# Kernel optimization log

Measured on AMD Instinct MI355X. Metric: run time of the kernel, lower is better.

## Reference

```python
import jax, jax.numpy as jnp
import numpy as np

NUM_STEPS = 5  # DVF2DDF(num_steps=5)


def _warp(vol, ddf, mode):
    """MONAI Warp: sample vol at (voxel index + ddf), align_corners=True, zeros padding.
    vol: [N,C,D,H,W]; ddf: [N,3,D,H,W] (channels = d,h,w displacement)."""
    N, C, D, H, W = vol.shape
    gd, gh, gw = jnp.meshgrid(jnp.arange(D, dtype=ddf.dtype),
                              jnp.arange(H, dtype=ddf.dtype),
                              jnp.arange(W, dtype=ddf.dtype), indexing='ij')
    cd = gd + ddf[:, 0]  # [N,D,H,W] absolute sample coords
    ch = gh + ddf[:, 1]
    cw = gw + ddf[:, 2]
    vol_flat = vol.reshape(N, C, D * H * W)

    def gather(di, hi, wi, valid):
        dc = jnp.clip(di, 0, D - 1)
        hc = jnp.clip(hi, 0, H - 1)
        wc = jnp.clip(wi, 0, W - 1)
        flat = ((dc * H + hc) * W + wc).reshape(N, 1, -1)
        v = jnp.take_along_axis(vol_flat, flat, axis=2).reshape(N, C, D, H, W)
        return v * valid[:, None]

    def in_bounds(di, hi, wi):
        return ((di >= 0) & (di < D) & (hi >= 0) & (hi < H)
                & (wi >= 0) & (wi < W)).astype(vol.dtype)

    if mode == 'nearest':
        di = jnp.round(cd).astype(jnp.int32)
        hi = jnp.round(ch).astype(jnp.int32)
        wi = jnp.round(cw).astype(jnp.int32)
        return gather(di, hi, wi, in_bounds(di, hi, wi))

    # trilinear ('bilinear' in grid_sample naming)
    d0 = jnp.floor(cd); h0 = jnp.floor(ch); w0 = jnp.floor(cw)
    fd = cd - d0; fh = ch - h0; fw = cw - w0
    d0i = d0.astype(jnp.int32); h0i = h0.astype(jnp.int32); w0i = w0.astype(jnp.int32)
    out = jnp.zeros_like(vol)
    for dd in (0, 1):
        for dh in (0, 1):
            for dw in (0, 1):
                di = d0i + dd; hi = h0i + dh; wi = w0i + dw
                wgt = ((fd if dd else 1 - fd)
                       * (fh if dh else 1 - fh)
                       * (fw if dw else 1 - fw))
                out = out + gather(di, hi, wi, in_bounds(di, hi, wi)) * wgt[:, None]
    return out


def _dvf2ddf(dvf, num_steps=NUM_STEPS):
    """Scaling-and-squaring integration of a stationary velocity field (MONAI DVF2DDF)."""
    ddf = dvf / (2 ** num_steps)
    for _ in range(num_steps):
        ddf = ddf + _warp(ddf, ddf, 'bilinear')
    return ddf


def setup_inputs() -> dict:
    key = jax.random.key(0)
    ks = jax.random.split(key, 6)
    D = H = W = 160
    return {
        "dvf0": jax.random.normal(ks[0], (1, 3, D, H, W), jnp.float32),
        "dvf1": jax.random.normal(ks[1], (1, 3, D, H, W), jnp.float32),
        "image": jax.random.normal(ks[2], (1, 1, D, H, W), jnp.float32),
        "cavity": jax.random.randint(ks[3], (1, 1, D, H, W), 0, 5, jnp.int32),
        "coronary": jax.random.randint(ks[4], (1, 1, D, H, W), 0, 3, jnp.int32),
        "w": jax.random.uniform(ks[5], (), jnp.float32),
    }


def reference(dvf0, dvf1, image, cavity, coronary, w):
    # linear blend of the two neighbouring phase DVFs
    dvf = dvf0 * (1 - w) + dvf1 * w
    ddf = _dvf2ddf(dvf)
    img_warped = _warp(image, ddf, 'bilinear')
    # labels are concatenated along batch and warped with nearest, ddf repeated
    labels = jnp.concatenate([cavity, coronary], axis=0).astype(jnp.float32)  # [2,1,D,H,W]
    lab_warped = _warp(labels, jnp.tile(ddf, (2, 1, 1, 1, 1)), 'nearest')
    cav_warped = lab_warped[0][None].astype(jnp.uint8)
    cor_warped = lab_warped[1][None].astype(jnp.uint8)
    return img_warped, cav_warped, cor_warped, ddf
```

## Files before the change

kernel.cpp:

```cpp
#include <hip/hip_runtime.h>

#define DD 160
#define HH 160
#define WW 160
#define PL (HH*WW)
#define S (DD*PL)

__device__ __forceinline__ float fmul(float a, float b){ return __fmul_rn(a,b); }
__device__ __forceinline__ float fadd(float a, float b){ return __fadd_rn(a,b); }
__device__ __forceinline__ float fsub(float a, float b){ return __fsub_rn(a,b); }

__global__ __launch_bounds__(256) void init_kernel(const float* __restrict__ dvf0,
                                                   const float* __restrict__ dvf1,
                                                   const float* __restrict__ wp,
                                                   float* __restrict__ outi) {
    int p = (blockIdx.x * 256 + threadIdx.x) * 4;
    float w = wp[0];
    float onew = fsub(1.0f, w);
    float a0[4], a1[4], a2[4], b0[4], b1[4], b2[4];
    *(float4*)a0 = *(const float4*)(dvf0 + p);
    *(float4*)a1 = *(const float4*)(dvf0 + S + p);
    *(float4*)a2 = *(const float4*)(dvf0 + 2 * S + p);
    *(float4*)b0 = *(const float4*)(dvf1 + p);
    *(float4*)b1 = *(const float4*)(dvf1 + S + p);
    *(float4*)b2 = *(const float4*)(dvf1 + 2 * S + p);
    float o[12];
    #pragma unroll
    for (int j = 0; j < 4; ++j) {
        o[3*j]   = fmul(fadd(fmul(a0[j], onew), fmul(b0[j], w)), 0.03125f);
        o[3*j+1] = fmul(fadd(fmul(a1[j], onew), fmul(b1[j], w)), 0.03125f);
        o[3*j+2] = fmul(fadd(fmul(a2[j], onew), fmul(b2[j], w)), 0.03125f);
    }
    float* dst = outi + (size_t)3 * p;
    *(float4*)(dst)     = *(float4*)(o);
    *(float4*)(dst + 4) = *(float4*)(o + 4);
    *(float4*)(dst + 8) = *(float4*)(o + 8);
}

template<bool PLANAR>
__global__ __launch_bounds__(256) void warp_step(const float* __restrict__ in,
                                                 float* __restrict__ out) {
    int b  = (blockIdx.x & 7) * 1000 + (blockIdx.x >> 3);
    int ix = b % 5;
    int r  = b / 5;
    int iy = r % 20;
    int iz = r / 20;
    int lane = threadIdx.x & 63, wid = threadIdx.x >> 6;
    int x  = (ix << 5) | (lane & 31);
    int y  = (iy << 3) | (wid << 1) | (lane >> 5);
    int z0 = iz << 1;
    int p0 = (z0 * HH + y) * WW + x;

    float ctr[2][3];
    #pragma unroll
    for (int j = 0; j < 2; ++j) {
        const float* src = in + (size_t)3 * (p0 + j * PL);
        ctr[j][0] = src[0]; ctr[j][1] = src[1]; ctr[j][2] = src[2];
    }

    #pragma unroll
    for (int j = 0; j < 2; ++j) {
        int z = z0 + j;
        int p = p0 + j * PL;
        float vd = ctr[j][0], vh = ctr[j][1], vw = ctr[j][2];
        float cd = fadd((float)z, vd);
        float ch = fadd((float)y, vh);
        float cw = fadd((float)x, vw);

        float d0 = floorf(cd), h0 = floorf(ch), w0 = floorf(cw);
        float fd = fsub(cd, d0), fh = fsub(ch, h0), fw = fsub(cw, w0);
        float gd = fsub(1.0f, fd), gh = fsub(1.0f, fh), gw = fsub(1.0f, fw);
        int d0i = (int)d0, h0i = (int)h0, w0i = (int)w0;

        int   qa[8];
        float wt[8];
        #pragma unroll
        for (int t = 0; t < 8; ++t) {
            int dd = t >> 2, dh = (t >> 1) & 1, dw = t & 1;
            int di = d0i + dd, hi = h0i + dh, wi = w0i + dw;
            bool valid = (di >= 0) & (di < DD) & (hi >= 0) & (hi < HH)
                       & (wi >= 0) & (wi < WW);
            float wgt = fmul(fmul(dd ? fd : gd, dh ? fh : gh), dw ? fw : gw);
            wt[t] = valid ? wgt : 0.0f;
            int dc = min(max(di, 0), DD - 1);
            int hc = min(max(hi, 0), HH - 1);
            int wc = min(max(wi, 0), WW - 1);
            qa[t] = 3 * ((dc * HH + hc) * WW + wc);
        }
        float g[8][3];
        #pragma unroll
        for (int t = 0; t < 8; ++t) {
            g[t][0] = in[qa[t]];
            g[t][1] = in[qa[t] + 1];
            g[t][2] = in[qa[t] + 2];
        }
        float acc0 = 0.0f, acc1 = 0.0f, acc2 = 0.0f;
        #pragma unroll
        for (int t = 0; t < 8; ++t) {
            acc0 = fadd(acc0, fmul(g[t][0], wt[t]));
            acc1 = fadd(acc1, fmul(g[t][1], wt[t]));
            acc2 = fadd(acc2, fmul(g[t][2], wt[t]));
        }
        float r0 = fadd(vd, acc0);
        float r1 = fadd(vh, acc1);
        float r2 = fadd(vw, acc2);

        if (PLANAR) {
            out[p] = r0; out[S + p] = r1; out[2 * S + p] = r2;
        } else {
            float* dst = out + (size_t)3 * p;
            dst[0] = r0; dst[1] = r1; dst[2] = r2;
        }
    }
}

__global__ __launch_bounds__(256) void final_kernel(const float* __restrict__ ddf,
                                                    const float* __restrict__ image,
                                                    const int* __restrict__ cav,
                                                    const int* __restrict__ cor,
                                                    float* __restrict__ out) {
    int b  = (blockIdx.x & 7) * 1000 + (blockIdx.x >> 3);
    int ix = b % 5;
    int r  = b / 5;
    int iy = r % 20;
    int iz = r / 20;
    int lane = threadIdx.x & 63, wid = threadIdx.x >> 6;
    int x  = (ix << 5) | (lane & 31);
    int y  = (iy << 3) | (wid << 1) | (lane >> 5);
    int z0 = iz << 1;
    int p0 = (z0 * HH + y) * WW + x;

    float dzs[2], dhs[2], dws[2];
    #pragma unroll
    for (int j = 0; j < 2; ++j) {
        dzs[j] = ddf[p0 + j * PL];
        dhs[j] = ddf[S + p0 + j * PL];
        dws[j] = ddf[2 * S + p0 + j * PL];
    }

    #pragma unroll
    for (int j = 0; j < 2; ++j) {
        int z = z0 + j;
        int p = p0 + j * PL;
        float cd = fadd((float)z, dzs[j]);
        float ch = fadd((float)y, dhs[j]);
        float cw = fadd((float)x, dws[j]);

        float d0 = floorf(cd), h0 = floorf(ch), w0 = floorf(cw);
        float fd = fsub(cd, d0), fh = fsub(ch, h0), fw = fsub(cw, w0);
        float gd = fsub(1.0f, fd), gh = fsub(1.0f, fh), gw = fsub(1.0f, fw);
        int d0i = (int)d0, h0i = (int)h0, w0i = (int)w0;

        int   qa[8];
        float wt[8];
        #pragma unroll
        for (int t = 0; t < 8; ++t) {
            int dd = t >> 2, dh = (t >> 1) & 1, dw = t & 1;
            int di = d0i + dd, hi = h0i + dh, wi = w0i + dw;
            bool valid = (di >= 0) & (di < DD) & (hi >= 0) & (hi < HH)
                       & (wi >= 0) & (wi < WW);
            float wgt = fmul(fmul(dd ? fd : gd, dh ? fh : gh), dw ? fw : gw);
            wt[t] = valid ? wgt : 0.0f;
            int dc = min(max(di, 0), DD - 1);
            int hc = min(max(hi, 0), HH - 1);
            int wc = min(max(wi, 0), WW - 1);
            qa[t] = (dc * HH + hc) * WW + wc;
        }
        float g[8];
        #pragma unroll
        for (int t = 0; t < 8; ++t) g[t] = image[qa[t]];
        float acc = 0.0f;
        #pragma unroll
        for (int t = 0; t < 8; ++t) acc = fadd(acc, fmul(g[t], wt[t]));
        out[p] = acc;

        int di = (int)rintf(cd), hi = (int)rintf(ch), wi = (int)rintf(cw);
        bool valid = (di >= 0) & (di < DD) & (hi >= 0) & (hi < HH)
                   & (wi >= 0) & (wi < WW);
        int dc = min(max(di, 0), DD - 1);
        int hc = min(max(hi, 0), HH - 1);
        int wc = min(max(wi, 0), WW - 1);
        int q = (dc * HH + hc) * WW + wc;
        out[S + p]     = valid ? (float)cav[q] : 0.0f;
        out[2 * S + p] = valid ? (float)cor[q] : 0.0f;
    }
}

extern "C" void kernel_launch(void* const* d_in, const int* in_sizes, int n_in,
                              void* d_out, int out_size, void* d_ws, size_t ws_size,
                              hipStream_t stream) {
    const float* dvf0   = (const float*)d_in[0];
    const float* dvf1   = (const float*)d_in[1];
    const float* image  = (const float*)d_in[2];
    const int*   cav    = (const int*)d_in[3];
    const int*   cor    = (const int*)d_in[4];
    const float* w      = (const float*)d_in[5];

    float* out  = (float*)d_out;
    float* bufA = out;
    float* bufB = out + (size_t)3 * S;

    init_kernel<<<4000, 256, 0, stream>>>(dvf0, dvf1, w, bufA);
    warp_step<false><<<8000, 256, 0, stream>>>(bufA, bufB);
    warp_step<false><<<8000, 256, 0, stream>>>(bufB, bufA);
    warp_step<false><<<8000, 256, 0, stream>>>(bufA, bufB);
    warp_step<false><<<8000, 256, 0, stream>>>(bufB, bufA);
    warp_step<true ><<<8000, 256, 0, stream>>>(bufA, bufB);
    final_kernel<<<8000, 256, 0, stream>>>(bufB, image, cav, cor, bufA);
}
```

Measured before the change: 412.5 us.

## Pad displacement field to float4 and pack image/labels for single gathers

Intermediate displacement fields are stored as padded float4 (AoS with a dummy lane) in workspace and output buffers, so each trilinear corner fetch is one 16-byte load instead of three scalar loads. The final warp packs image, cavity and coronary into a float4 volume, so one gather serves both trilinear image sampling and nearest label lookup. The nearest label is chosen from the eight trilinear corners by comparing the rounded index with the floor index. This costs extra workspace, a pack pass, and a third more bytes per voxel. If the workspace is too small, the old path is used.

```diff
diff --git a/kernel.cpp b/kernel.cpp
--- a/kernel.cpp
+++ b/kernel.cpp
@@ -9,6 +9,188 @@
 __device__ __forceinline__ float fmul(float a, float b){ return __fmul_rn(a,b); }
 __device__ __forceinline__ float fadd(float a, float b){ return __fadd_rn(a,b); }
 __device__ __forceinline__ float fsub(float a, float b){ return __fsub_rn(a,b); }
+
+
+__global__ __launch_bounds__(256) void init4_kernel(const float* __restrict__ dvf0,
+                                                    const float* __restrict__ dvf1,
+                                                    const float* __restrict__ wp,
+                                                    float4* __restrict__ outi) {
+    int p = (blockIdx.x * 256 + threadIdx.x) * 4;
+    float w = wp[0];
+    float onew = fsub(1.0f, w);
+    float a0[4], a1[4], a2[4], b0[4], b1[4], b2[4];
+    *(float4*)a0 = *(const float4*)(dvf0 + p);
+    *(float4*)a1 = *(const float4*)(dvf0 + S + p);
+    *(float4*)a2 = *(const float4*)(dvf0 + 2 * S + p);
+    *(float4*)b0 = *(const float4*)(dvf1 + p);
+    *(float4*)b1 = *(const float4*)(dvf1 + S + p);
+    *(float4*)b2 = *(const float4*)(dvf1 + 2 * S + p);
+    #pragma unroll
+    for (int j = 0; j < 4; ++j) {
+        float o0 = fmul(fadd(fmul(a0[j], onew), fmul(b0[j], w)), 0.03125f);
+        float o1 = fmul(fadd(fmul(a1[j], onew), fmul(b1[j], w)), 0.03125f);
+        float o2 = fmul(fadd(fmul(a2[j], onew), fmul(b2[j], w)), 0.03125f);
+        outi[p + j] = make_float4(o0, o1, o2, 0.0f);
+    }
+}
+
+template<bool PLANAR>
+__global__ __launch_bounds__(256) void warp_step4(const float4* __restrict__ in,
+                                                  float4* __restrict__ out4,
+                                                  float* __restrict__ outp) {
+    int b  = (blockIdx.x & 7) * 1000 + (blockIdx.x >> 3);
+    int ix = b % 5;
+    int r  = b / 5;
+    int iy = r % 20;
+    int iz = r / 20;
+    int lane = threadIdx.x & 63, wid = threadIdx.x >> 6;
+    int x  = (ix << 5) | (lane & 31);
+    int y  = (iy << 3) | (wid << 1) | (lane >> 5);
+    int z0 = iz << 1;
+    int p0 = (z0 * HH + y) * WW + x;
+
+    float4 ctr[2];
+    ctr[0] = in[p0];
+    ctr[1] = in[p0 + PL];
+
+    #pragma unroll
+    for (int j = 0; j < 2; ++j) {
+        int z = z0 + j;
+        int p = p0 + j * PL;
+        float vd = ctr[j].x, vh = ctr[j].y, vw = ctr[j].z;
+        float cd = fadd((float)z, vd);
+        float ch = fadd((float)y, vh);
+        float cw = fadd((float)x, vw);
+
+        float d0 = floorf(cd), h0 = floorf(ch), w0 = floorf(cw);
+        float fd = fsub(cd, d0), fh = fsub(ch, h0), fw = fsub(cw, w0);
+        float gd = fsub(1.0f, fd), gh = fsub(1.0f, fh), gw = fsub(1.0f, fw);
+        int d0i = (int)d0, h0i = (int)h0, w0i = (int)w0;
+
+        int   qa[8];
+        float wt[8];
+        #pragma unroll
+        for (int t = 0; t < 8; ++t) {
+            int dd = t >> 2, dh = (t >> 1) & 1, dw = t & 1;
+            int di = d0i + dd, hi = h0i + dh, wi = w0i + dw;
+            bool valid = (di >= 0) & (di < DD) & (hi >= 0) & (hi < HH)
+                       & (wi >= 0) & (wi < WW);
+            float wgt = fmul(fmul(dd ? fd : gd, dh ? fh : gh), dw ? fw : gw);
+            wt[t] = valid ? wgt : 0.0f;
+            int dc = min(max(di, 0), DD - 1);
+            int hc = min(max(hi, 0), HH - 1);
+            int wc = min(max(wi, 0), WW - 1);
+            qa[t] = (dc * HH + hc) * WW + wc;
+        }
+        float4 g[8];
+        #pragma unroll
+        for (int t = 0; t < 8; ++t) g[t] = in[qa[t]];
+
+        float acc0 = 0.0f, acc1 = 0.0f, acc2 = 0.0f;
+        #pragma unroll
+        for (int t = 0; t < 8; ++t) {
+            acc0 = fadd(acc0, fmul(g[t].x, wt[t]));
+            acc1 = fadd(acc1, fmul(g[t].y, wt[t]));
+            acc2 = fadd(acc2, fmul(g[t].z, wt[t]));
+        }
+        float r0 = fadd(vd, acc0);
+        float r1 = fadd(vh, acc1);
+        float r2 = fadd(vw, acc2);
+
+        if (PLANAR) {
+            outp[p] = r0; outp[S + p] = r1; outp[2 * S + p] = r2;
+        } else {
+            out4[p] = make_float4(r0, r1, r2, 0.0f);
+        }
+    }
+}
+
+__global__ __launch_bounds__(256) void pack_kernel(const float* __restrict__ img,
+                                                   const int* __restrict__ cav,
+                                                   const int* __restrict__ cor,
+                                                   float4* __restrict__ out) {
+    int p = (blockIdx.x * 256 + threadIdx.x) * 4;
+    float im[4]; int cv[4]; int co[4];
+    *(float4*)im = *(const float4*)(img + p);
+    *(int4*)cv   = *(const int4*)(cav + p);
+    *(int4*)co   = *(const int4*)(cor + p);
+    #pragma unroll
+    for (int j = 0; j < 4; ++j)
+        out[p + j] = make_float4(im[j], (float)cv[j], (float)co[j], 0.0f);
+}
+
+__global__ __launch_bounds__(256) void final4_kernel(const float* __restrict__ ddf,
+                                                     const float4* __restrict__ packed,
+                                                     float* __restrict__ out) {
+    int b  = (blockIdx.x & 7) * 1000 + (blockIdx.x >> 3);
+    int ix = b % 5;
+    int r  = b / 5;
+    int iy = r % 20;
+    int iz = r / 20;
+    int lane = threadIdx.x & 63, wid = threadIdx.x >> 6;
+    int x  = (ix << 5) | (lane & 31);
+    int y  = (iy << 3) | (wid << 1) | (lane >> 5);
+    int z0 = iz << 1;
+    int p0 = (z0 * HH + y) * WW + x;
+
+    float dzs[2], dhs[2], dws[2];
+    #pragma unroll
+    for (int j = 0; j < 2; ++j) {
+        dzs[j] = ddf[p0 + j * PL];
+        dhs[j] = ddf[S + p0 + j * PL];
+        dws[j] = ddf[2 * S + p0 + j * PL];
+    }
+
+    #pragma unroll
+    for (int j = 0; j < 2; ++j) {
+        int z = z0 + j;
+        int p = p0 + j * PL;
+        float cd = fadd((float)z, dzs[j]);
+        float ch = fadd((float)y, dhs[j]);
+        float cw = fadd((float)x, dws[j]);
+
+        float d0 = floorf(cd), h0 = floorf(ch), w0 = floorf(cw);
+        float fd = fsub(cd, d0), fh = fsub(ch, h0), fw = fsub(cw, w0);
+        float gd = fsub(1.0f, fd), gh = fsub(1.0f, fh), gw = fsub(1.0f, fw);
+        int d0i = (int)d0, h0i = (int)h0, w0i = (int)w0;
+
+        int   qa[8];
+        float wt[8];
+        #pragma unroll
+        for (int t = 0; t < 8; ++t) {
+            int dd = t >> 2, dh = (t >> 1) & 1, dw = t & 1;
+            int di = d0i + dd, hi = h0i + dh, wi = w0i + dw;
+            bool valid = (di >= 0) & (di < DD) & (hi >= 0) & (hi < HH)
+                       & (wi >= 0) & (wi < WW);
+            float wgt = fmul(fmul(dd ? fd : gd, dh ? fh : gh), dw ? fw : gw);
+            wt[t] = valid ? wgt : 0.0f;
+            int dc = min(max(di, 0), DD - 1);
+            int hc = min(max(hi, 0), HH - 1);
+            int wc = min(max(wi, 0), WW - 1);
+            qa[t] = (dc * HH + hc) * WW + wc;
+        }
+        float4 g[8];
+        #pragma unroll
+        for (int t = 0; t < 8; ++t) g[t] = packed[qa[t]];
+
+        float acc = 0.0f;
+        #pragma unroll
+        for (int t = 0; t < 8; ++t) acc = fadd(acc, fmul(g[t].x, wt[t]));
+        out[p] = acc;
+
+        int rd = (int)rintf(cd), rh = (int)rintf(ch), rw = (int)rintf(cw);
+        bool vn = (rd >= 0) & (rd < DD) & (rh >= 0) & (rh < HH)
+                & (rw >= 0) & (rw < WW);
+        bool b2 = (rd != d0i), b1 = (rh != h0i), b0 = (rw != w0i);
+        float cavv = b2 ? (b1 ? (b0 ? g[7].y : g[6].y) : (b0 ? g[5].y : g[4].y))
+                        : (b1 ? (b0 ? g[3].y : g[2].y) : (b0 ? g[1].y : g[0].y));
+        float corv = b2 ? (b1 ? (b0 ? g[7].z : g[6].z) : (b0 ? g[5].z : g[4].z))
+                        : (b1 ? (b0 ? g[3].z : g[2].z) : (b0 ? g[1].z : g[0].z));
+        out[S + p]     = vn ? cavv : 0.0f;
+        out[2 * S + p] = vn ? corv : 0.0f;
+    }
+}
+
 
 __global__ __launch_bounds__(256) void init_kernel(const float* __restrict__ dvf0,
                                                    const float* __restrict__ dvf1,
@@ -196,15 +378,31 @@
     const int*   cor    = (const int*)d_in[4];
     const float* w      = (const float*)d_in[5];
 
-    float* out  = (float*)d_out;
-    float* bufA = out;
-    float* bufB = out + (size_t)3 * S;
-
-    init_kernel<<<4000, 256, 0, stream>>>(dvf0, dvf1, w, bufA);
-    warp_step<false><<<8000, 256, 0, stream>>>(bufA, bufB);
-    warp_step<false><<<8000, 256, 0, stream>>>(bufB, bufA);
-    warp_step<false><<<8000, 256, 0, stream>>>(bufA, bufB);
-    warp_step<false><<<8000, 256, 0, stream>>>(bufB, bufA);
-    warp_step<true ><<<8000, 256, 0, stream>>>(bufA, bufB);
-    final_kernel<<<8000, 256, 0, stream>>>(bufB, image, cav, cor, bufA);
-}
+    float* out = (float*)d_out;
+
+    const size_t need = (size_t)4 * S * sizeof(float);
+    if (ws_size >= need) {
+        float4* A = (float4*)d_ws;
+        float4* B = (float4*)d_out;
+        float*  ddf_planar = out + (size_t)3 * S;
+
+        init4_kernel<<<4000, 256, 0, stream>>>(dvf0, dvf1, w, A);
+        warp_step4<false><<<8000, 256, 0, stream>>>(A, B, nullptr);
+        warp_step4<false><<<8000, 256, 0, stream>>>(B, A, nullptr);
+        warp_step4<false><<<8000, 256, 0, stream>>>(A, B, nullptr);
+        warp_step4<false><<<8000, 256, 0, stream>>>(B, A, nullptr);
+        warp_step4<true ><<<8000, 256, 0, stream>>>(A, nullptr, ddf_planar);
+        pack_kernel<<<4000, 256, 0, stream>>>(image, cav, cor, A);
+        final4_kernel<<<8000, 256, 0, stream>>>(ddf_planar, A, out);
+    } else {
+        float* bufA = out;
+        float* bufB = out + (size_t)3 * S;
+        init_kernel<<<4000, 256, 0, stream>>>(dvf0, dvf1, w, bufA);
+        warp_step<false><<<8000, 256, 0, stream>>>(bufA, bufB);
+        warp_step<false><<<8000, 256, 0, stream>>>(bufB, bufA);
+        warp_step<false><<<8000, 256, 0, stream>>>(bufA, bufB);
+        warp_step<false><<<8000, 256, 0, stream>>>(bufB, bufA);
+        warp_step<true ><<<8000, 256, 0, stream>>>(bufA, bufB);
+        final_kernel<<<8000, 256, 0, stream>>>(bufB, image, cav, cor, bufA);
+    }
+}
```

After: 439.6 us. +6.6%, slower.
